# Kernel optimization log

Hardware: AMD Instinct MI355X
Metric: run time of the kernel (lower is better)

Reference implementation:

```python
import jax, jax.numpy as jnp
import numpy as np

N, E, IN_DIM, HID, HEADS, OUT_DIM, N_GRAPHS = 50000, 640000, 128, 64, 8, 2, 64
NEG_SLOPE = 0.2  # PyG GATConv default leaky_relu slope


def setup_inputs() -> dict:
    key = jax.random.key(0)
    ks = jax.random.split(key, 12)
    x = jax.random.normal(ks[0], (N, IN_DIM), jnp.float32)
    edge_index = jax.random.randint(ks[1], (2, E), 0, N, jnp.int32)
    batch = jnp.sort(jax.random.randint(ks[2], (N,), 0, N_GRAPHS, jnp.int32))
    def glorot(k, shape):
        fan_in = shape[0]
        return jax.random.normal(k, shape, jnp.float32) / np.sqrt(fan_in)
    return {
        "x": x,
        "W1": glorot(ks[3], (IN_DIM, HEADS * HID)),
        "att_src1": glorot(ks[4], (HEADS, HID)),
        "att_dst1": glorot(ks[5], (HEADS, HID)),
        "b1": jnp.zeros((HEADS * HID,), jnp.float32),
        "W2": glorot(ks[6], (HEADS * HID, HID)),
        "att_src2": glorot(ks[7], (1, HID)),
        "att_dst2": glorot(ks[8], (1, HID)),
        "b2": jnp.zeros((HID,), jnp.float32),
        "fc_w": glorot(ks[9], (HID, OUT_DIM)),
        "fc_b": jnp.zeros((OUT_DIM,), jnp.float32),
        "edge_index": edge_index,
        "batch": batch,
    }


def gat_layer(x, src, dst, W, a_src, a_dst, bias):
    # PyG GATConv: h = x @ W per head; alpha_e = LeakyReLU(a_src.h_src + a_dst.h_dst),
    # softmax over edges sharing the same dst, weighted scatter-sum, concat heads.
    H, C = a_src.shape
    h = (x @ W).reshape(-1, H, C)                       # [N, H, C]
    a_s = jnp.einsum('nhc,hc->nh', h, a_src)            # [N, H]
    a_d = jnp.einsum('nhc,hc->nh', h, a_dst)
    e = jax.nn.leaky_relu(a_s[src] + a_d[dst], NEG_SLOPE)  # [Etot, H]
    e_max = jax.ops.segment_max(e, dst, num_segments=N)
    e = jnp.exp(e - e_max[dst])
    denom = jax.ops.segment_sum(e, dst, num_segments=N)
    alpha = e / (denom[dst] + 1e-16)                    # edge softmax
    msg = h[src] * alpha[..., None]                     # [Etot, H, C]
    out = jax.ops.segment_sum(msg, dst, num_segments=N) # [N, H, C]
    return out.reshape(-1, H * C) + bias


def reference(x, W1, att_src1, att_dst1, b1, W2, att_src2, att_dst2, b2, fc_w, fc_b, edge_index, batch):
    # add self-loops (PyG GATConv default add_self_loops=True)
    loop = jnp.arange(N, dtype=edge_index.dtype)
    src = jnp.concatenate([edge_index[0], loop])
    dst = jnp.concatenate([edge_index[1], loop])

    h = gat_layer(x, src, dst, W1, att_src1, att_dst1, b1)   # [N, HEADS*HID]
    h = jax.nn.elu(h)
    # dropout is identity at eval
    h = gat_layer(h, src, dst, W2, att_src2, att_dst2, b2)   # [N, HID]
    h = jax.nn.elu(h)

    # global mean pool over graphs
    sums = jax.ops.segment_sum(h, batch, num_segments=N_GRAPHS)
    cnts = jax.ops.segment_sum(jnp.ones((N, 1), h.dtype), batch, num_segments=N_GRAPHS)
    pooled = sums / jnp.maximum(cnts, 1.0)                   # [G, HID]
    return pooled @ fc_w + fc_b                              # [G, OUT_DIM]
```

## Files before the change

### kernel.cpp

```cpp
#include <hip/hip_runtime.h>
#include <hip/hip_bf16.h>
#include <cstdint>
#include <cstddef>

#define N_NODES   50000
#define N_EDGES   640000
#define ETOT      (N_EDGES + N_NODES)
#define IN_DIM    128
#define HID       64
#define HEADS     8
#define F1        (HEADS * HID)
#define OUT_DIM   2
#define N_GRAPHS  64
#define NEG_SLOPE 0.2f
#define CAP       64

typedef __attribute__((ext_vector_type(8))) short s8v;
typedef __attribute__((ext_vector_type(4))) float f32x4;
typedef unsigned char uchar;
typedef unsigned int  uint;

__device__ __forceinline__ float leakyf(float x) { return x > 0.f ? x : NEG_SLOPE * x; }
__device__ __forceinline__ float eluf(float x)   { return x > 0.f ? x : __expf(x) - 1.f; }

__device__ __forceinline__ float bf2f(ushort u) {
    union { uint32_t i; float f; } c; c.i = ((uint32_t)u) << 16; return c.f;
}
__device__ __forceinline__ ushort f2bf(float f) {
    union { float f; uint32_t i; } c; c.f = f;
    uint32_t r = c.i + 0x7FFFu + ((c.i >> 16) & 1u);
    return (ushort)(r >> 16);
}
template<int SEL>
__device__ __forceinline__ float fp8f(uint w) {
    return __builtin_amdgcn_cvt_f32_fp8(w, SEL);
}
__device__ __forceinline__ uchar f2fp8(float f) {
    uint p = __builtin_amdgcn_cvt_pk_fp8_f32(f, f, 0u, false);
    return (uchar)(p & 0xFFu);
}

#define XW_ITEMS  (N_NODES * IN_DIM / 4)
#define W1_ITEMS  (F1 * IN_DIM)
#define W2_ITEMS  (HID * F1)
#define PREP_ITEMS (ETOT + XW_ITEMS + W1_ITEMS + W2_ITEMS)

__global__ __launch_bounds__(256) void prep_fill(const int* __restrict__ srcI,
                                                 const int* __restrict__ dstI,
                                                 int* __restrict__ counts,
                                                 int* __restrict__ csrp,
                                                 const float* __restrict__ x,
                                                 const float* __restrict__ W1,
                                                 const float* __restrict__ W2,
                                                 ushort* __restrict__ xb,
                                                 ushort* __restrict__ W1T,
                                                 ushort* __restrict__ W2T) {
    int i = blockIdx.x * 256 + threadIdx.x;
    if (i < ETOT) {
        int s, d;
        if (i < N_EDGES) { s = srcI[i]; d = dstI[i]; }
        else             { s = d = i - N_EDGES; }
        int slot = atomicAdd(&counts[d], 1);
        if (slot < CAP) csrp[d * CAP + slot] = s;
    } else if (i < ETOT + XW_ITEMS) {
        int idx = i - ETOT;
        float4 v = *reinterpret_cast<const float4*>(x + (size_t)idx * 4);
        ushort4 u;
        u.x = f2bf(v.x); u.y = f2bf(v.y); u.z = f2bf(v.z); u.w = f2bf(v.w);
        *reinterpret_cast<ushort4*>(xb + (size_t)idx * 4) = u;
    } else if (i < ETOT + XW_ITEMS + W1_ITEMS) {
        int idx = i - ETOT - XW_ITEMS;
        int n = idx >> 7, k = idx & 127;
        W1T[idx] = f2bf(W1[(size_t)k * F1 + n]);
    } else if (i < PREP_ITEMS) {
        int idx = i - ETOT - XW_ITEMS - W1_ITEMS;
        int n = idx >> 9, k = idx & 511;
        W2T[idx] = f2bf(W2[(size_t)k * HID + n]);
    }
}

template<int BM, int BN, int BK, int AH>
__global__ __launch_bounds__(256) void gemm_att(const ushort* __restrict__ A,
                                                const ushort* __restrict__ BT,
                                                uchar* __restrict__ C8,
                                                int M, int N, int K,
                                                const float* __restrict__ att_s,
                                                const float* __restrict__ att_d,
                                                float* __restrict__ as_o,
                                                float* __restrict__ ad_o,
                                                ushort* __restrict__ Cb) {
    __shared__ ushort As[BM * BK];
    __shared__ ushort Bs[BN * BK];
    const int t    = threadIdx.x;
    const int row0 = blockIdx.y * BM;
    const int col0 = blockIdx.x * BN;
    const int lane = t & 63;
    const int wr   = t >> 6;
    constexpr int FR = BM / 64;

    f32x4 acc[FR][4];
    #pragma unroll
    for (int i = 0; i < FR; ++i)
        #pragma unroll
        for (int j = 0; j < 4; ++j)
            acc[i][j] = (f32x4){0.f, 0.f, 0.f, 0.f};

    constexpr int A_IT = BM * BK / 8 / 256;
    constexpr int B_IT = BN * BK / 8 / 256;

    for (int k0 = 0; k0 < K; k0 += BK) {
        #pragma unroll
        for (int i = 0; i < A_IT; ++i) {
            int ch  = t + 256 * i;
            int r   = ch >> 3;
            int c16 = ch & 7;
            uint4 v = make_uint4(0u, 0u, 0u, 0u);
            int gr = row0 + r;
            if (gr < M)
                v = *reinterpret_cast<const uint4*>(A + (size_t)gr * K + k0 + c16 * 8);
            int off = (ch * 16) ^ ((r & 7) << 4);
            *reinterpret_cast<uint4*>(reinterpret_cast<char*>(As) + off) = v;
        }
        #pragma unroll
        for (int i = 0; i < B_IT; ++i) {
            int ch  = t + 256 * i;
            int r   = ch >> 3;
            int c16 = ch & 7;
            uint4 v = *reinterpret_cast<const uint4*>(BT + (size_t)(col0 + r) * K + k0 + c16 * 8);
            int off = (ch * 16) ^ ((r & 7) << 4);
            *reinterpret_cast<uint4*>(reinterpret_cast<char*>(Bs) + off) = v;
        }
        __syncthreads();
        #pragma unroll
        for (int kk = 0; kk < BK; kk += 32) {
            s8v af[FR], bf[4];
            #pragma unroll
            for (int fr = 0; fr < FR; ++fr) {
                int r   = wr * (FR * 16) + fr * 16 + (lane & 15);
                int off = (r * (BK * 2) + kk * 2 + (lane >> 4) * 16) ^ ((r & 7) << 4);
                af[fr] = *reinterpret_cast<const s8v*>(reinterpret_cast<const char*>(As) + off);
            }
            #pragma unroll
            for (int fc = 0; fc < 4; ++fc) {
                int r   = fc * 16 + (lane & 15);
                int off = (r * (BK * 2) + kk * 2 + (lane >> 4) * 16) ^ ((r & 7) << 4);
                bf[fc] = *reinterpret_cast<const s8v*>(reinterpret_cast<const char*>(Bs) + off);
            }
            #pragma unroll
            for (int fr = 0; fr < FR; ++fr)
                #pragma unroll
                for (int fc = 0; fc < 4; ++fc)
                    acc[fr][fc] = __builtin_amdgcn_mfma_f32_16x16x32_bf16(af[fr], bf[fc], acc[fr][fc], 0, 0, 0);
        }
        __syncthreads();
    }

    float avs[4], avd[4];
    const float* asp = att_s + blockIdx.x * BN;
    const float* adp = att_d + blockIdx.x * BN;
    #pragma unroll
    for (int fc = 0; fc < 4; ++fc) {
        avs[fc] = asp[fc * 16 + (lane & 15)];
        avd[fc] = adp[fc * 16 + (lane & 15)];
    }

    #pragma unroll
    for (int fr = 0; fr < FR; ++fr) {
        #pragma unroll
        for (int j = 0; j < 4; ++j) {
            int row = row0 + wr * (FR * 16) + fr * 16 + (lane >> 4) * 4 + j;
            if (row < M) {
                float sv = 0.f, dv = 0.f;
                #pragma unroll
                for (int fc = 0; fc < 4; ++fc) {
                    float c = acc[fr][fc][j];
                    int col = col0 + fc * 16 + (lane & 15);
                    C8[(size_t)row * N + col] = f2fp8(c);
                    if (Cb) Cb[(size_t)row * N + col] = f2bf(c);
                    sv = fmaf(c, avs[fc], sv);
                    dv = fmaf(c, avd[fc], dv);
                }
                #pragma unroll
                for (int off = 1; off < 16; off <<= 1) {
                    sv += __shfl_xor(sv, off);
                    dv += __shfl_xor(dv, off);
                }
                if ((lane & 15) == 0) {
                    as_o[(size_t)row * AH + blockIdx.x] = sv;
                    ad_o[(size_t)row * AH + blockIdx.x] = dv;
                }
            }
        }
    }
}

__global__ __launch_bounds__(256) void gat_agg1(const uchar* __restrict__ h8,
                                                const float* __restrict__ as,
                                                const float* __restrict__ ad,
                                                const int* __restrict__ counts,
                                                const int* __restrict__ csrp,
                                                const float* __restrict__ bias,
                                                ushort* __restrict__ z) {
    __shared__ float lds_w[4][HEADS][CAP + 1];
    int tid  = threadIdx.x;
    int wid  = tid >> 6;
    int dst  = (blockIdx.x * 256 + tid) >> 6;
    int lane = tid & 63;
    if (dst >= N_NODES) return;
    int cnt = min(counts[dst], CAP);
    int hd  = lane >> 3;

    int myidx = (lane < cnt) ? csrp[(size_t)dst * CAP + lane] : 0;
    float4 a0 = *reinterpret_cast<const float4*>(as + (size_t)myidx * HEADS);
    float4 a1 = *reinterpret_cast<const float4*>(as + (size_t)myidx * HEADS + 4);
    float4 d0 = *reinterpret_cast<const float4*>(ad + (size_t)dst * HEADS);
    float4 d1 = *reinterpret_cast<const float4*>(ad + (size_t)dst * HEADS + 4);
    lds_w[wid][0][lane] = __expf(leakyf(a0.x + d0.x));
    lds_w[wid][1][lane] = __expf(leakyf(a0.y + d0.y));
    lds_w[wid][2][lane] = __expf(leakyf(a0.z + d0.z));
    lds_w[wid][3][lane] = __expf(leakyf(a0.w + d0.w));
    lds_w[wid][4][lane] = __expf(leakyf(a1.x + d1.x));
    lds_w[wid][5][lane] = __expf(leakyf(a1.y + d1.y));
    lds_w[wid][6][lane] = __expf(leakyf(a1.z + d1.z));
    lds_w[wid][7][lane] = __expf(leakyf(a1.w + d1.w));

    float accv[8] = {0.f, 0.f, 0.f, 0.f, 0.f, 0.f, 0.f, 0.f};
    float den = 0.f;
    const uchar* hb = h8 + (size_t)lane * 8;
    for (int j0 = 0; j0 < cnt; j0 += 4) {
        int n = cnt - j0;
        int s0 = 0, s1 = 0, s2 = 0, s3 = 0;
        uint2 v0 = {}, v1 = {}, v2 = {}, v3 = {};
        float w0 = 0.f, w1 = 0.f, w2 = 0.f, w3 = 0.f;
        s0 = __shfl(myidx, j0);
        v0 = *reinterpret_cast<const uint2*>(hb + (size_t)s0 * F1);
        w0 = lds_w[wid][hd][j0];
        if (n > 1) {
            s1 = __shfl(myidx, j0 + 1);
            v1 = *reinterpret_cast<const uint2*>(hb + (size_t)s1 * F1);
            w1 = lds_w[wid][hd][j0 + 1];
        }
        if (n > 2) {
            s2 = __shfl(myidx, j0 + 2);
            v2 = *reinterpret_cast<const uint2*>(hb + (size_t)s2 * F1);
            w2 = lds_w[wid][hd][j0 + 2];
        }
        if (n > 3) {
            s3 = __shfl(myidx, j0 + 3);
            v3 = *reinterpret_cast<const uint2*>(hb + (size_t)s3 * F1);
            w3 = lds_w[wid][hd][j0 + 3];
        }
        {
            den += w0;
            accv[0] = fmaf(w0, fp8f<0>(v0.x), accv[0]);
            accv[1] = fmaf(w0, fp8f<1>(v0.x), accv[1]);
            accv[2] = fmaf(w0, fp8f<2>(v0.x), accv[2]);
            accv[3] = fmaf(w0, fp8f<3>(v0.x), accv[3]);
            accv[4] = fmaf(w0, fp8f<0>(v0.y), accv[4]);
            accv[5] = fmaf(w0, fp8f<1>(v0.y), accv[5]);
            accv[6] = fmaf(w0, fp8f<2>(v0.y), accv[6]);
            accv[7] = fmaf(w0, fp8f<3>(v0.y), accv[7]);
        }
        if (n > 1) {
            den += w1;
            accv[0] = fmaf(w1, fp8f<0>(v1.x), accv[0]);
            accv[1] = fmaf(w1, fp8f<1>(v1.x), accv[1]);
            accv[2] = fmaf(w1, fp8f<2>(v1.x), accv[2]);
            accv[3] = fmaf(w1, fp8f<3>(v1.x), accv[3]);
            accv[4] = fmaf(w1, fp8f<0>(v1.y), accv[4]);
            accv[5] = fmaf(w1, fp8f<1>(v1.y), accv[5]);
            accv[6] = fmaf(w1, fp8f<2>(v1.y), accv[6]);
            accv[7] = fmaf(w1, fp8f<3>(v1.y), accv[7]);
        }
        if (n > 2) {
            den += w2;
            accv[0] = fmaf(w2, fp8f<0>(v2.x), accv[0]);
            accv[1] = fmaf(w2, fp8f<1>(v2.x), accv[1]);
            accv[2] = fmaf(w2, fp8f<2>(v2.x), accv[2]);
            accv[3] = fmaf(w2, fp8f<3>(v2.x), accv[3]);
            accv[4] = fmaf(w2, fp8f<0>(v2.y), accv[4]);
            accv[5] = fmaf(w2, fp8f<1>(v2.y), accv[5]);
            accv[6] = fmaf(w2, fp8f<2>(v2.y), accv[6]);
            accv[7] = fmaf(w2, fp8f<3>(v2.y), accv[7]);
        }
        if (n > 3) {
            den += w3;
            accv[0] = fmaf(w3, fp8f<0>(v3.x), accv[0]);
            accv[1] = fmaf(w3, fp8f<1>(v3.x), accv[1]);
            accv[2] = fmaf(w3, fp8f<2>(v3.x), accv[2]);
            accv[3] = fmaf(w3, fp8f<3>(v3.x), accv[3]);
            accv[4] = fmaf(w3, fp8f<0>(v3.y), accv[4]);
            accv[5] = fmaf(w3, fp8f<1>(v3.y), accv[5]);
            accv[6] = fmaf(w3, fp8f<2>(v3.y), accv[6]);
            accv[7] = fmaf(w3, fp8f<3>(v3.y), accv[7]);
        }
    }
    float inv = 1.f / (den + 1e-16f);
    s8v ov;
    #pragma unroll
    for (int c = 0; c < 8; ++c) {
        float v = accv[c] * inv + bias[lane * 8 + c];
        ov[c] = (short)f2bf(eluf(v));
    }
    *reinterpret_cast<s8v*>(z + (size_t)dst * F1 + lane * 8) = ov;
}

__global__ __launch_bounds__(256) void gat_agg2(const uchar* __restrict__ h8,
                                                const float* __restrict__ as,
                                                const float* __restrict__ ad,
                                                const int* __restrict__ counts,
                                                const int* __restrict__ csrp,
                                                const float* __restrict__ bias,
                                                float* __restrict__ z) {
    int dst  = (blockIdx.x * 256 + threadIdx.x) >> 6;
    int lane = threadIdx.x & 63;
    if (dst >= N_NODES) return;
    int cnt = min(counts[dst], CAP);
    float adv = ad[dst];

    int myidx = (lane < cnt) ? csrp[(size_t)dst * CAP + lane] : 0;
    float wl  = (lane < cnt) ? __expf(leakyf(as[myidx] + adv)) : 0.f;
    float den = wl;
    #pragma unroll
    for (int off = 32; off > 0; off >>= 1) den += __shfl_xor(den, off);

    float acc = 0.f;
    for (int j0 = 0; j0 < cnt; j0 += 4) {
        int n = cnt - j0;
        int s0 = 0, s1 = 0, s2 = 0, s3 = 0;
        float w0 = 0.f, w1 = 0.f, w2 = 0.f, w3 = 0.f;
        uint b0 = 0, b1 = 0, b2 = 0, b3 = 0;
        s0 = __shfl(myidx, j0);     w0 = __shfl(wl, j0);
        b0 = h8[(size_t)s0 * HID + lane];
        if (n > 1) { s1 = __shfl(myidx, j0 + 1); w1 = __shfl(wl, j0 + 1); b1 = h8[(size_t)s1 * HID + lane]; }
        if (n > 2) { s2 = __shfl(myidx, j0 + 2); w2 = __shfl(wl, j0 + 2); b2 = h8[(size_t)s2 * HID + lane]; }
        if (n > 3) { s3 = __shfl(myidx, j0 + 3); w3 = __shfl(wl, j0 + 3); b3 = h8[(size_t)s3 * HID + lane]; }
        acc = fmaf(w0, fp8f<0>(b0), acc);
        if (n > 1) acc = fmaf(w1, fp8f<0>(b1), acc);
        if (n > 2) acc = fmaf(w2, fp8f<0>(b2), acc);
        if (n > 3) acc = fmaf(w3, fp8f<0>(b3), acc);
    }
    float v = acc / (den + 1e-16f) + bias[lane];
    z[(size_t)dst * HID + lane] = eluf(v);
}

__global__ __launch_bounds__(256) void pool_fc(const float* __restrict__ z,
                                               const int* __restrict__ batch,
                                               const float* __restrict__ fc_w,
                                               const float* __restrict__ fc_b,
                                               float* __restrict__ out) {
    int g = blockIdx.x;
    int t = threadIdx.x, lane = t & 63, w = t >> 6;
    auto lb = [&](int key) {
        int lo = 0, hi = N_NODES;
        while (lo < hi) { int mid = (lo + hi) >> 1; if (batch[mid] < key) lo = mid + 1; else hi = mid; }
        return lo;
    };
    int lo = lb(g), hi = lb(g + 1);
    float acc = 0.f;
    for (int n = lo + w; n < hi; n += 4)
        acc += z[(size_t)n * HID + lane];
    __shared__ float sh[4][HID];
    sh[w][lane] = acc;
    __syncthreads();
    if (w == 0) {
        float s = sh[0][lane] + sh[1][lane] + sh[2][lane] + sh[3][lane];
        float cntf = fmaxf((float)(hi - lo), 1.f);
        float mean = s / cntf;
        float p0 = mean * fc_w[lane * OUT_DIM + 0];
        float p1 = mean * fc_w[lane * OUT_DIM + 1];
        #pragma unroll
        for (int off = 32; off > 0; off >>= 1) {
            p0 += __shfl_xor(p0, off);
            p1 += __shfl_xor(p1, off);
        }
        if (lane == 0) {
            out[g * OUT_DIM + 0] = p0 + fc_b[0];
            out[g * OUT_DIM + 1] = p1 + fc_b[1];
        }
    }
}

extern "C" void kernel_launch(void* const* d_in, const int* in_sizes, int n_in,
                              void* d_out, int out_size, void* d_ws, size_t ws_size,
                              hipStream_t stream) {
    const float* x    = (const float*)d_in[0];
    const float* W1   = (const float*)d_in[1];
    const float* at_s1= (const float*)d_in[2];
    const float* at_d1= (const float*)d_in[3];
    const float* b1   = (const float*)d_in[4];
    const float* W2   = (const float*)d_in[5];
    const float* at_s2= (const float*)d_in[6];
    const float* at_d2= (const float*)d_in[7];
    const float* b2   = (const float*)d_in[8];
    const float* fcw  = (const float*)d_in[9];
    const float* fcb  = (const float*)d_in[10];
    const int*   ei   = (const int*)d_in[11];
    const int*   batch= (const int*)d_in[12];
    float* out = (float*)d_out;

    char* p = (char*)d_ws;
    auto alloc = [&](size_t bytes) {
        char* r = p;
        p += (bytes + 255) & ~size_t(255);
        return r;
    };
    int*    counts= (int*)alloc((size_t)N_NODES * 4);
    ushort* xb    = (ushort*)alloc((size_t)N_NODES * IN_DIM * 2);
    ushort* W1T   = (ushort*)alloc((size_t)F1 * IN_DIM * 2);
    ushort* W2T   = (ushort*)alloc((size_t)HID * F1 * 2);
    uchar*  h1    = (uchar*)alloc((size_t)N_NODES * F1);
    ushort* z1    = (ushort*)alloc((size_t)N_NODES * F1 * 2);
    uchar*  h2    = (uchar*)alloc((size_t)N_NODES * HID);
    float*  z2    = (float*)alloc((size_t)N_NODES * HID * 4);
    float*  as1   = (float*)alloc((size_t)N_NODES * HEADS * 4);
    float*  ad1   = (float*)alloc((size_t)N_NODES * HEADS * 4);
    float*  as2   = (float*)alloc((size_t)N_NODES * 4);
    float*  ad2   = (float*)alloc((size_t)N_NODES * 4);
    int*    csrp  = (int*)alloc((size_t)N_NODES * CAP * 4);

    const int* srcI = ei;
    const int* dstI = ei + N_EDGES;

    (void)hipMemsetAsync(counts, 0, (size_t)N_NODES * 4, stream);

    prep_fill<<<(PREP_ITEMS + 255) / 256, 256, 0, stream>>>(
        srcI, dstI, counts, csrp, x, W1, W2, xb, W1T, W2T);

    dim3 g1(F1 / 64, (N_NODES + 127) / 128);
    gemm_att<128, 64, 64, HEADS><<<g1, 256, 0, stream>>>(
        xb, W1T, h1, N_NODES, F1, IN_DIM, at_s1, at_d1, as1, ad1, (ushort*)nullptr);
    gat_agg1<<<(N_NODES + 3) / 4, 256, 0, stream>>>(h1, as1, ad1, counts, csrp, b1, z1);

    dim3 g2(1, (N_NODES + 63) / 64);
    gemm_att<64, 64, 64, 1><<<g2, 256, 0, stream>>>(
        z1, W2T, h2, N_NODES, HID, F1, at_s2, at_d2, as2, ad2, (ushort*)nullptr);
    gat_agg2<<<(N_NODES + 3) / 4, 256, 0, stream>>>(h2, as2, ad2, counts, csrp, b2, z2);

    pool_fc<<<N_GRAPHS, 256, 0, stream>>>(z2, batch, fcw, fcb, out);
}
```

Baseline: 328.7 us.

## Shrink CSR indices to u16, remap GEMM blocks per XCD, pack fp8 unpack, widen pool

Several unrelated changes land together. CSR source indices are stored as 16-bit values, halving neighbour-list traffic. The GEMM grid is flattened and remapped so neighbouring tiles land on the same XCD for L2 reuse, and the unused bf16 output path is dropped. The layer-1 aggregation uses packed fp8-to-f32x2 conversion with vector FMAs, and pool_fc uses 512 threads with four accumulators per thread. Node ids up to 50000 fit in u16, but this ties the code to the node count.

```diff
diff --git a/kernel.cpp b/kernel.cpp
--- a/kernel.cpp
+++ b/kernel.cpp
@@ -17,6 +17,7 @@
 
 typedef __attribute__((ext_vector_type(8))) short s8v;
 typedef __attribute__((ext_vector_type(4))) float f32x4;
+typedef __attribute__((ext_vector_type(2))) float f32x2;
 typedef unsigned char uchar;
 typedef unsigned int  uint;
 
@@ -35,6 +36,10 @@
 __device__ __forceinline__ float fp8f(uint w) {
     return __builtin_amdgcn_cvt_f32_fp8(w, SEL);
 }
+template<bool HI>
+__device__ __forceinline__ f32x2 pk8(uint w) {
+    return __builtin_amdgcn_cvt_pk_f32_fp8(w, HI);
+}
 __device__ __forceinline__ uchar f2fp8(float f) {
     uint p = __builtin_amdgcn_cvt_pk_fp8_f32(f, f, 0u, false);
     return (uchar)(p & 0xFFu);
@@ -48,7 +53,7 @@
 __global__ __launch_bounds__(256) void prep_fill(const int* __restrict__ srcI,
                                                  const int* __restrict__ dstI,
                                                  int* __restrict__ counts,
-                                                 int* __restrict__ csrp,
+                                                 ushort* __restrict__ csrp,
                                                  const float* __restrict__ x,
                                                  const float* __restrict__ W1,
                                                  const float* __restrict__ W2,
@@ -61,7 +66,7 @@
         if (i < N_EDGES) { s = srcI[i]; d = dstI[i]; }
         else             { s = d = i - N_EDGES; }
         int slot = atomicAdd(&counts[d], 1);
-        if (slot < CAP) csrp[d * CAP + slot] = s;
+        if (slot < CAP) csrp[d * CAP + slot] = (ushort)s;
     } else if (i < ETOT + XW_ITEMS) {
         int idx = i - ETOT;
         float4 v = *reinterpret_cast<const float4*>(x + (size_t)idx * 4);
@@ -87,13 +92,21 @@
                                                 const float* __restrict__ att_s,
                                                 const float* __restrict__ att_d,
                                                 float* __restrict__ as_o,
-                                                float* __restrict__ ad_o,
-                                                ushort* __restrict__ Cb) {
+                                                float* __restrict__ ad_o) {
+    int nwg = gridDim.x;
+    int q = nwg >> 3, r = nwg & 7;
+    int xcd = blockIdx.x & 7, loc = blockIdx.x >> 3;
+    int sid = (xcd < r) ? (xcd * (q + 1) + loc)
+                        : (r * (q + 1) + (xcd - r) * q + loc);
+    int ncb = N / BN;
+    int bx = sid % ncb;
+    int by = sid / ncb;
+
     __shared__ ushort As[BM * BK];
     __shared__ ushort Bs[BN * BK];
     const int t    = threadIdx.x;
-    const int row0 = blockIdx.y * BM;
-    const int col0 = blockIdx.x * BN;
+    const int row0 = by * BM;
+    const int col0 = bx * BN;
     const int lane = t & 63;
     const int wr   = t >> 6;
     constexpr int FR = BM / 64;
@@ -112,22 +125,22 @@
         #pragma unroll
         for (int i = 0; i < A_IT; ++i) {
             int ch  = t + 256 * i;
-            int r   = ch >> 3;
+            int rr  = ch >> 3;
             int c16 = ch & 7;
             uint4 v = make_uint4(0u, 0u, 0u, 0u);
-            int gr = row0 + r;
+            int gr = row0 + rr;
             if (gr < M)
                 v = *reinterpret_cast<const uint4*>(A + (size_t)gr * K + k0 + c16 * 8);
-            int off = (ch * 16) ^ ((r & 7) << 4);
+            int off = (ch * 16) ^ ((rr & 7) << 4);
             *reinterpret_cast<uint4*>(reinterpret_cast<char*>(As) + off) = v;
         }
         #pragma unroll
         for (int i = 0; i < B_IT; ++i) {
             int ch  = t + 256 * i;
-            int r   = ch >> 3;
+            int rr  = ch >> 3;
             int c16 = ch & 7;
-            uint4 v = *reinterpret_cast<const uint4*>(BT + (size_t)(col0 + r) * K + k0 + c16 * 8);
-            int off = (ch * 16) ^ ((r & 7) << 4);
+            uint4 v = *reinterpret_cast<const uint4*>(BT + (size_t)(col0 + rr) * K + k0 + c16 * 8);
+            int off = (ch * 16) ^ ((rr & 7) << 4);
             *reinterpret_cast<uint4*>(reinterpret_cast<char*>(Bs) + off) = v;
         }
         __syncthreads();
@@ -136,14 +149,14 @@
             s8v af[FR], bf[4];
             #pragma unroll
             for (int fr = 0; fr < FR; ++fr) {
-                int r   = wr * (FR * 16) + fr * 16 + (lane & 15);
-                int off = (r * (BK * 2) + kk * 2 + (lane >> 4) * 16) ^ ((r & 7) << 4);
+                int rr  = wr * (FR * 16) + fr * 16 + (lane & 15);
+                int off = (rr * (BK * 2) + kk * 2 + (lane >> 4) * 16) ^ ((rr & 7) << 4);
                 af[fr] = *reinterpret_cast<const s8v*>(reinterpret_cast<const char*>(As) + off);
             }
             #pragma unroll
             for (int fc = 0; fc < 4; ++fc) {
-                int r   = fc * 16 + (lane & 15);
-                int off = (r * (BK * 2) + kk * 2 + (lane >> 4) * 16) ^ ((r & 7) << 4);
+                int rr  = fc * 16 + (lane & 15);
+                int off = (rr * (BK * 2) + kk * 2 + (lane >> 4) * 16) ^ ((rr & 7) << 4);
                 bf[fc] = *reinterpret_cast<const s8v*>(reinterpret_cast<const char*>(Bs) + off);
             }
             #pragma unroll
@@ -156,8 +169,8 @@
     }
 
     float avs[4], avd[4];
-    const float* asp = att_s + blockIdx.x * BN;
-    const float* adp = att_d + blockIdx.x * BN;
+    const float* asp = att_s + bx * BN;
+    const float* adp = att_d + bx * BN;
     #pragma unroll
     for (int fc = 0; fc < 4; ++fc) {
         avs[fc] = asp[fc * 16 + (lane & 15)];
@@ -176,7 +189,6 @@
                     float c = acc[fr][fc][j];
                     int col = col0 + fc * 16 + (lane & 15);
                     C8[(size_t)row * N + col] = f2fp8(c);
-                    if (Cb) Cb[(size_t)row * N + col] = f2bf(c);
                     sv = fmaf(c, avs[fc], sv);
                     dv = fmaf(c, avd[fc], dv);
                 }
@@ -186,8 +198,8 @@
                     dv += __shfl_xor(dv, off);
                 }
                 if ((lane & 15) == 0) {
-                    as_o[(size_t)row * AH + blockIdx.x] = sv;
-                    ad_o[(size_t)row * AH + blockIdx.x] = dv;
+                    as_o[(size_t)row * AH + bx] = sv;
+                    ad_o[(size_t)row * AH + bx] = dv;
                 }
             }
         }
@@ -198,7 +210,7 @@
                                                 const float* __restrict__ as,
                                                 const float* __restrict__ ad,
                                                 const int* __restrict__ counts,
-                                                const int* __restrict__ csrp,
+                                                const ushort* __restrict__ csrp,
                                                 const float* __restrict__ bias,
                                                 ushort* __restrict__ z) {
     __shared__ float lds_w[4][HEADS][CAP + 1];
@@ -210,7 +222,7 @@
     int cnt = min(counts[dst], CAP);
     int hd  = lane >> 3;
 
-    int myidx = (lane < cnt) ? csrp[(size_t)dst * CAP + lane] : 0;
+    int myidx = (lane < cnt) ? (int)csrp[(size_t)dst * CAP + lane] : 0;
     float4 a0 = *reinterpret_cast<const float4*>(as + (size_t)myidx * HEADS);
     float4 a1 = *reinterpret_cast<const float4*>(as + (size_t)myidx * HEADS + 4);
     float4 d0 = *reinterpret_cast<const float4*>(ad + (size_t)dst * HEADS);
@@ -224,7 +236,9 @@
     lds_w[wid][6][lane] = __expf(leakyf(a1.z + d1.z));
     lds_w[wid][7][lane] = __expf(leakyf(a1.w + d1.w));
 
-    float accv[8] = {0.f, 0.f, 0.f, 0.f, 0.f, 0.f, 0.f, 0.f};
+    f32x2 acc2[4];
+    acc2[0] = (f32x2){0.f, 0.f}; acc2[1] = (f32x2){0.f, 0.f};
+    acc2[2] = (f32x2){0.f, 0.f}; acc2[3] = (f32x2){0.f, 0.f};
     float den = 0.f;
     const uchar* hb = h8 + (size_t)lane * 8;
     for (int j0 = 0; j0 < cnt; j0 += 4) {
@@ -251,55 +265,43 @@
             w3 = lds_w[wid][hd][j0 + 3];
         }
         {
+            f32x2 wv = (f32x2){w0, w0};
             den += w0;
-            accv[0] = fmaf(w0, fp8f<0>(v0.x), accv[0]);
-            accv[1] = fmaf(w0, fp8f<1>(v0.x), accv[1]);
-            accv[2] = fmaf(w0, fp8f<2>(v0.x), accv[2]);
-            accv[3] = fmaf(w0, fp8f<3>(v0.x), accv[3]);
-            accv[4] = fmaf(w0, fp8f<0>(v0.y), accv[4]);
-            accv[5] = fmaf(w0, fp8f<1>(v0.y), accv[5]);
-            accv[6] = fmaf(w0, fp8f<2>(v0.y), accv[6]);
-            accv[7] = fmaf(w0, fp8f<3>(v0.y), accv[7]);
+            acc2[0] += pk8<false>(v0.x) * wv;
+            acc2[1] += pk8<true >(v0.x) * wv;
+            acc2[2] += pk8<false>(v0.y) * wv;
+            acc2[3] += pk8<true >(v0.y) * wv;
         }
         if (n > 1) {
+            f32x2 wv = (f32x2){w1, w1};
             den += w1;
-            accv[0] = fmaf(w1, fp8f<0>(v1.x), accv[0]);
-            accv[1] = fmaf(w1, fp8f<1>(v1.x), accv[1]);
-            accv[2] = fmaf(w1, fp8f<2>(v1.x), accv[2]);
-            accv[3] = fmaf(w1, fp8f<3>(v1.x), accv[3]);
-            accv[4] = fmaf(w1, fp8f<0>(v1.y), accv[4]);
-            accv[5] = fmaf(w1, fp8f<1>(v1.y), accv[5]);
-            accv[6] = fmaf(w1, fp8f<2>(v1.y), accv[6]);
-            accv[7] = fmaf(w1, fp8f<3>(v1.y), accv[7]);
+            acc2[0] += pk8<false>(v1.x) * wv;
+            acc2[1] += pk8<true >(v1.x) * wv;
+            acc2[2] += pk8<false>(v1.y) * wv;
+            acc2[3] += pk8<true >(v1.y) * wv;
         }
         if (n > 2) {
+            f32x2 wv = (f32x2){w2, w2};
             den += w2;
-            accv[0] = fmaf(w2, fp8f<0>(v2.x), accv[0]);
-            accv[1] = fmaf(w2, fp8f<1>(v2.x), accv[1]);
-            accv[2] = fmaf(w2, fp8f<2>(v2.x), accv[2]);
-            accv[3] = fmaf(w2, fp8f<3>(v2.x), accv[3]);
-            accv[4] = fmaf(w2, fp8f<0>(v2.y), accv[4]);
-            accv[5] = fmaf(w2, fp8f<1>(v2.y), accv[5]);
-            accv[6] = fmaf(w2, fp8f<2>(v2.y), accv[6]);
-            accv[7] = fmaf(w2, fp8f<3>(v2.y), accv[7]);
+            acc2[0] += pk8<false>(v2.x) * wv;
+            acc2[1] += pk8<true >(v2.x) * wv;
+            acc2[2] += pk8<false>(v2.y) * wv;
+            acc2[3] += pk8<true >(v2.y) * wv;
         }
         if (n > 3) {
+            f32x2 wv = (f32x2){w3, w3};
             den += w3;
-            accv[0] = fmaf(w3, fp8f<0>(v3.x), accv[0]);
-            accv[1] = fmaf(w3, fp8f<1>(v3.x), accv[1]);
-            accv[2] = fmaf(w3, fp8f<2>(v3.x), accv[2]);
-            accv[3] = fmaf(w3, fp8f<3>(v3.x), accv[3]);
-            accv[4] = fmaf(w3, fp8f<0>(v3.y), accv[4]);
-            accv[5] = fmaf(w3, fp8f<1>(v3.y), accv[5]);
-            accv[6] = fmaf(w3, fp8f<2>(v3.y), accv[6]);
-            accv[7] = fmaf(w3, fp8f<3>(v3.y), accv[7]);
+            acc2[0] += pk8<false>(v3.x) * wv;
+            acc2[1] += pk8<true >(v3.x) * wv;
+            acc2[2] += pk8<false>(v3.y) * wv;
+            acc2[3] += pk8<true >(v3.y) * wv;
         }
     }
     float inv = 1.f / (den + 1e-16f);
     s8v ov;
     #pragma unroll
     for (int c = 0; c < 8; ++c) {
-        float v = accv[c] * inv + bias[lane * 8 + c];
+        float v = acc2[c >> 1][c & 1] * inv + bias[lane * 8 + c];
         ov[c] = (short)f2bf(eluf(v));
     }
     *reinterpret_cast<s8v*>(z + (size_t)dst * F1 + lane * 8) = ov;
@@ -309,7 +311,7 @@
                                                 const float* __restrict__ as,
                                                 const float* __restrict__ ad,
                                                 const int* __restrict__ counts,
-                                                const int* __restrict__ csrp,
+                                                const ushort* __restrict__ csrp,
                                                 const float* __restrict__ bias,
                                                 float* __restrict__ z) {
     int dst  = (blockIdx.x * 256 + threadIdx.x) >> 6;
@@ -318,7 +320,7 @@
     int cnt = min(counts[dst], CAP);
     float adv = ad[dst];
 
-    int myidx = (lane < cnt) ? csrp[(size_t)dst * CAP + lane] : 0;
+    int myidx = (lane < cnt) ? (int)csrp[(size_t)dst * CAP + lane] : 0;
     float wl  = (lane < cnt) ? __expf(leakyf(as[myidx] + adv)) : 0.f;
     float den = wl;
     #pragma unroll
@@ -344,7 +346,7 @@
     z[(size_t)dst * HID + lane] = eluf(v);
 }
 
-__global__ __launch_bounds__(256) void pool_fc(const float* __restrict__ z,
+__global__ __launch_bounds__(512) void pool_fc(const float* __restrict__ z,
                                                const int* __restrict__ batch,
                                                const float* __restrict__ fc_w,
                                                const float* __restrict__ fc_b,
@@ -357,14 +359,21 @@
         return lo;
     };
     int lo = lb(g), hi = lb(g + 1);
-    float acc = 0.f;
-    for (int n = lo + w; n < hi; n += 4)
-        acc += z[(size_t)n * HID + lane];
-    __shared__ float sh[4][HID];
+    float a0 = 0.f, a1 = 0.f, a2 = 0.f, a3 = 0.f;
+    for (int n0 = lo + (w << 2); n0 < hi; n0 += 32) {
+        a0 += z[(size_t)n0 * HID + lane];
+        if (n0 + 1 < hi) a1 += z[(size_t)(n0 + 1) * HID + lane];
+        if (n0 + 2 < hi) a2 += z[(size_t)(n0 + 2) * HID + lane];
+        if (n0 + 3 < hi) a3 += z[(size_t)(n0 + 3) * HID + lane];
+    }
+    float acc = (a0 + a1) + (a2 + a3);
+    __shared__ float sh[8][HID];
     sh[w][lane] = acc;
     __syncthreads();
     if (w == 0) {
-        float s = sh[0][lane] + sh[1][lane] + sh[2][lane] + sh[3][lane];
+        float s = 0.f;
+        #pragma unroll
+        for (int i = 0; i < 8; ++i) s += sh[i][lane];
         float cntf = fmaxf((float)(hi - lo), 1.f);
         float mean = s / cntf;
         float p0 = mean * fc_w[lane * OUT_DIM + 0];
@@ -417,7 +426,7 @@
     float*  ad1   = (float*)alloc((size_t)N_NODES * HEADS * 4);
     float*  as2   = (float*)alloc((size_t)N_NODES * 4);
     float*  ad2   = (float*)alloc((size_t)N_NODES * 4);
-    int*    csrp  = (int*)alloc((size_t)N_NODES * CAP * 4);
+    ushort* csrp  = (ushort*)alloc((size_t)N_NODES * CAP * 2);
 
     const int* srcI = ei;
     const int* dstI = ei + N_EDGES;
@@ -427,15 +436,15 @@
     prep_fill<<<(PREP_ITEMS + 255) / 256, 256, 0, stream>>>(
         srcI, dstI, counts, csrp, x, W1, W2, xb, W1T, W2T);
 
-    dim3 g1(F1 / 64, (N_NODES + 127) / 128);
-    gemm_att<128, 64, 64, HEADS><<<g1, 256, 0, stream>>>(
-        xb, W1T, h1, N_NODES, F1, IN_DIM, at_s1, at_d1, as1, ad1, (ushort*)nullptr);
+    int nwg1 = (F1 / 64) * ((N_NODES + 127) / 128);
+    gemm_att<128, 64, 64, HEADS><<<nwg1, 256, 0, stream>>>(
+        xb, W1T, h1, N_NODES, F1, IN_DIM, at_s1, at_d1, as1, ad1);
     gat_agg1<<<(N_NODES + 3) / 4, 256, 0, stream>>>(h1, as1, ad1, counts, csrp, b1, z1);
 
-    dim3 g2(1, (N_NODES + 63) / 64);
-    gemm_att<64, 64, 64, 1><<<g2, 256, 0, stream>>>(
-        z1, W2T, h2, N_NODES, HID, F1, at_s2, at_d2, as2, ad2, (ushort*)nullptr);
+    int nwg2 = 1 * ((N_NODES + 63) / 64);
+    gemm_att<64, 64, 64, 1><<<nwg2, 256, 0, stream>>>(
+        z1, W2T, h2, N_NODES, HID, F1, at_s2, at_d2, as2, ad2);
     gat_agg2<<<(N_NODES + 3) / 4, 256, 0, stream>>>(h2, as2, ad2, counts, csrp, b2, z2);
 
-    pool_fc<<<N_GRAPHS, 256, 0, stream>>>(z2, batch, fcw, fcb, out);
-}
+    pool_fc<<<N_GRAPHS, 512, 0, stream>>>(z2, batch, fcw, fcb, out);
+}
```

Result: faster. 285.4 us (-13.2%).
